# Kernel optimization log

Hardware: AMD Instinct MI355X
Metric: run time of the kernel (lower is better)

Reference implementation:

```python
import jax, jax.numpy as jnp
import numpy as np

INF = 1e38  # matches torch module's INF = 1e+38


def setup_inputs() -> dict:
    key = jax.random.key(0)
    k1, k2, k3 = jax.random.split(key, 3)
    n_len, batch, dim = 2048, 4, 512
    # scale query so QK^T logits don't fully saturate the softmax
    query = jax.random.normal(k1, (n_len, batch, dim), dtype=jnp.float32) * 0.05
    W_in = jax.random.normal(k2, (dim, dim), dtype=jnp.float32) * (1.0 / np.sqrt(dim))
    W_out = jax.random.normal(k3, (dim, 2 * dim), dtype=jnp.float32) * (1.0 / np.sqrt(2 * dim))
    return {"query": query, "W_in": W_in, "W_out": W_out}


def reference(query, W_in, W_out):
    # query: [n_len, batch, dim]; torch .t() swaps first two dims -> [batch, n_len, dim]
    q = jnp.transpose(query, (1, 0, 2))
    b, n, d = q.shape
    # attention_type == 'general': linear_in (no bias), y = x @ W^T
    q = jnp.einsum('bnd,ed->bne', q, W_in)
    # scores: [b, n, n]
    scores = jnp.einsum('bnd,bmd->bnm', q, q)
    # mask = triu(ones) INCLUDING diagonal -> set to -INF (row 0 fully masked)
    mask = jnp.triu(jnp.ones((n, n), dtype=bool))
    scores = jnp.where(mask[None, :, :], -INF, scores)
    weights = jax.nn.softmax(scores, axis=-1)  # row 0 becomes uniform (all -INF)
    # manual zero-out of row 0 of the attention weights
    weights = weights.at[:, 0, :].set(0.0)
    mix = jnp.einsum('bnm,bmd->bnd', weights, q)
    combined = jnp.concatenate([mix, q], axis=-1)  # [b, n, 2d]
    out = jnp.einsum('bnk,dk->bnd', combined, W_out)  # linear_out, no bias
    out = jax.nn.selu(out)
    # final .t() -> [n_len, batch, dim]
    return jnp.transpose(out, (1, 0, 2)), weights
```

## Files before the change

kernel.cpp:

```cpp
#include <hip/hip_runtime.h>
#include <hip/hip_bf16.h>

typedef unsigned short u16;
typedef unsigned int u32;

#define BATCH 4
#define NLEN 2048
#define DIM 512
#define LDSK 40

typedef __attribute__((ext_vector_type(8))) __bf16 bf16x8;
typedef __attribute__((ext_vector_type(4))) float f32x4;

__device__ __forceinline__ u16 f32_to_bf16(float f) {
  union { float f; u32 u; } v; v.f = f;
  u32 u = v.u;
  return (u16)((u + 0x7FFFu + ((u >> 16) & 1u)) >> 16);
}
__device__ __forceinline__ u32 pk2(float lo, float hi) {
  return (u32)f32_to_bf16(lo) | ((u32)f32_to_bf16(hi) << 16);
}
__device__ __forceinline__ void stage8_f32(u16* dst, const float* src) {
  float4 a = *(const float4*)src;
  float4 b = *(const float4*)(src + 4);
  uint4 o;
  o.x = pk2(a.x, a.y); o.y = pk2(a.z, a.w);
  o.z = pk2(b.x, b.y); o.w = pk2(b.z, b.w);
  *(uint4*)dst = o;
}
__device__ __forceinline__ void stage16_f32(u16* dst, const float* src) {
  stage8_f32(dst, src); stage8_f32(dst + 8, src + 8);
}
__device__ __forceinline__ void stage8_bf16(u16* dst, const u16* src) {
  *(uint4*)dst = *(const uint4*)src;
}
__device__ __forceinline__ void stage16_bf16(u16* dst, const u16* src) {
  *(uint4*)dst = *(const uint4*)src;
  *(uint4*)(dst + 8) = *(const uint4*)(src + 8);
}
__device__ __forceinline__ void stage8_sum(u16* dst, const u16* s0, const u16* s1,
                                           const u16* s2, int cnt) {
  uint4 a = *(const uint4*)s0;
  u32 wa[4] = {a.x, a.y, a.z, a.w};
  float v[8];
#pragma unroll
  for (int i = 0; i < 4; ++i) {
    v[2 * i] = __uint_as_float(wa[i] << 16);
    v[2 * i + 1] = __uint_as_float(wa[i] & 0xffff0000u);
  }
  if (cnt > 1) {
    uint4 bq = *(const uint4*)s1;
    u32 wb[4] = {bq.x, bq.y, bq.z, bq.w};
#pragma unroll
    for (int i = 0; i < 4; ++i) {
      v[2 * i] += __uint_as_float(wb[i] << 16);
      v[2 * i + 1] += __uint_as_float(wb[i] & 0xffff0000u);
    }
  }
  if (cnt > 2) {
    uint4 cq = *(const uint4*)s2;
    u32 wc[4] = {cq.x, cq.y, cq.z, cq.w};
#pragma unroll
    for (int i = 0; i < 4; ++i) {
      v[2 * i] += __uint_as_float(wc[i] << 16);
      v[2 * i + 1] += __uint_as_float(wc[i] & 0xffff0000u);
    }
  }
  uint4 o;
  o.x = pk2(v[0], v[1]); o.y = pk2(v[2], v[3]);
  o.z = pk2(v[4], v[5]); o.w = pk2(v[6], v[7]);
  *(uint4*)dst = o;
}

template <int MR, int NR>
__device__ __forceinline__ void mma_tile(const u16* As, const u16* Bs, f32x4 acc[MR][NR],
                                         int wm, int wn, int lr, int lk) {
  bf16x8 af[MR], bfr[NR];
#pragma unroll
  for (int m = 0; m < MR; ++m)
    af[m] = *(const bf16x8*)(As + (wm + m * 16 + lr) * LDSK + lk);
#pragma unroll
  for (int n = 0; n < NR; ++n)
    bfr[n] = *(const bf16x8*)(Bs + (wn + n * 16 + lr) * LDSK + lk);
#pragma unroll
  for (int m = 0; m < MR; ++m)
#pragma unroll
    for (int n = 0; n < NR; ++n)
      acc[m][n] = __builtin_amdgcn_mfma_f32_16x16x32_bf16(af[m], bfr[n], acc[m][n], 0, 0, 0);
}

__global__ __launch_bounds__(256) void k_qproj(const float* __restrict__ query,
                                               const float* __restrict__ W_in,
                                               u16* __restrict__ qp, u16* __restrict__ qt) {
  __shared__ u16 As[64 * LDSK];
  __shared__ u16 Bs[128 * LDSK];
  __shared__ u16 tbuf[128][72];
  const int t = threadIdx.x;
  const int lane = t & 63, wid = t >> 6;
  const int wm = (wid >> 1) * 32, wn = (wid & 1) * 64;
  const int lr = lane & 15, lk = (lane >> 4) * 8;
  const int trow4 = t >> 2, tseg = (t & 3) * 8;
  const int trow2 = t >> 1, thalf = (t & 1) * 16;
  const int rbase = blockIdx.y * 64;
  const int cbase = blockIdx.x * 128;
  const int rg = rbase + trow4;
  const int bb = rg >> 11, nn = rg & 2047;
  const float* aRow = query + (size_t)(nn * BATCH + bb) * DIM + tseg;
  const float* bRow = W_in + (size_t)(cbase + trow2) * DIM + thalf;
  f32x4 acc[2][4] = {};
  for (int k0 = 0; k0 < DIM; k0 += 32) {
    stage8_f32(As + trow4 * LDSK + tseg, aRow + k0);
    stage16_f32(Bs + trow2 * LDSK + thalf, bRow + k0);
    __syncthreads();
    mma_tile<2, 4>(As, Bs, acc, wm, wn, lr, lk);
    __syncthreads();
  }
#pragma unroll
  for (int m = 0; m < 2; ++m)
#pragma unroll
    for (int n = 0; n < 4; ++n)
#pragma unroll
      for (int j = 0; j < 4; ++j) {
        int rl = wm + m * 16 + (lane >> 4) * 4 + j;
        int cl = wn + n * 16 + lr;
        u16 v = f32_to_bf16(acc[m][n][j]);
        qp[(size_t)(rbase + rl) * DIM + cbase + cl] = v;
        tbuf[cl][rl] = v;
      }
  __syncthreads();
  const int bb0 = rbase >> 11, nbase = rbase & 2047;
#pragma unroll
  for (int i = 0; i < 4; ++i) {
    int idx = t + i * 256;
    int dl = idx >> 3, c = idx & 7;
    uint4 v = *(const uint4*)&tbuf[dl][c * 8];
    *(uint4*)(qt + (size_t)(bb0 * DIM + cbase + dl) * NLEN + nbase + c * 8) = v;
  }
}

__global__ __launch_bounds__(256) void k_scores(const u16* __restrict__ qp,
                                                u16* __restrict__ swf) {
  const int mt = blockIdx.x;
  const int nt = blockIdx.y;
  const int b = blockIdx.z;
  if (mt > (nt >> 1)) return;
  __shared__ u16 As[64 * LDSK];
  __shared__ u16 Bs[128 * LDSK];
  const int t = threadIdx.x;
  const int lane = t & 63, wid = t >> 6;
  const int wm = (wid >> 1) * 32, wn = (wid & 1) * 64;
  const int lr = lane & 15, lk = (lane >> 4) * 8;
  const int trow4 = t >> 2, tseg = (t & 3) * 8;
  const int trow2 = t >> 1, thalf = (t & 1) * 16;
  const u16* aRow = qp + (size_t)(b * NLEN + nt * 64 + trow4) * DIM + tseg;
  const u16* bRow = qp + (size_t)(b * NLEN + mt * 128 + trow2) * DIM + thalf;
  f32x4 acc[2][4] = {};
  for (int k0 = 0; k0 < DIM; k0 += 32) {
    stage8_bf16(As + trow4 * LDSK + tseg, aRow + k0);
    stage16_bf16(Bs + trow2 * LDSK + thalf, bRow + k0);
    __syncthreads();
    mma_tile<2, 4>(As, Bs, acc, wm, wn, lr, lk);
    __syncthreads();
  }
  const int NT = nt >> 1;
  u16* wtile = swf + ((size_t)(b * 136 + NT * (NT + 1) / 2 + mt) << 14);
  const int rowoff = (nt & 1) * 64;
#pragma unroll
  for (int m = 0; m < 2; ++m)
#pragma unroll
    for (int n = 0; n < 4; ++n)
#pragma unroll
      for (int j = 0; j < 4; ++j) {
        int rl = wm + m * 16 + (lane >> 4) * 4 + j;
        int cl = wn + n * 16 + lr;
        wtile[(rowoff + rl) * 128 + cl] = f32_to_bf16(acc[m][n][j]);
      }
}

__global__ __launch_bounds__(256) void k_softmax(u16* __restrict__ swf, float* __restrict__ w) {
  const int n = blockIdx.x, b = blockIdx.y;
  const int t = threadIdx.x;
  float* wrow = w + ((size_t)b * NLEN + n) * NLEN;
  const int nt = n >> 7;
  const size_t tb = ((size_t)(b * 136 + nt * (nt + 1) / 2) << 14) + ((size_t)(n & 127) << 7);
  __shared__ float srow[NLEN];
  __shared__ float red[4];
  if (n == 0) {
    for (int i = t; i < NLEN / 4; i += 256) ((float4*)wrow)[i] = float4{0, 0, 0, 0};
    if (t < 16) ((uint4*)(swf + tb))[t] = uint4{0, 0, 0, 0};
    return;
  }
  const int lane = t & 63, wid = t >> 6;
  const int nchunk = (nt + 1) * 16;
  float mx = -1e38f;
  for (int idx = t; idx < nchunk; idx += 256) {
    const int mt = idx >> 4, c = idx & 15;
    uint4 rv = *(const uint4*)(swf + tb + ((size_t)mt << 14) + c * 8);
    int m0 = mt * 128 + c * 8;
    u32 wds[4] = {rv.x, rv.y, rv.z, rv.w};
#pragma unroll
    for (int wi = 0; wi < 4; ++wi) {
      float v0 = __uint_as_float(wds[wi] << 16);
      float v1 = __uint_as_float(wds[wi] & 0xffff0000u);
      int m = m0 + wi * 2;
      srow[m] = v0; srow[m + 1] = v1;
      if (m < n) mx = fmaxf(mx, v0);
      if (m + 1 < n) mx = fmaxf(mx, v1);
    }
  }
#pragma unroll
  for (int off = 32; off; off >>= 1) mx = fmaxf(mx, __shfl_xor(mx, off));
  if (lane == 0) red[wid] = mx;
  __syncthreads();
  mx = fmaxf(fmaxf(red[0], red[1]), fmaxf(red[2], red[3]));
  float sum = 0.f;
  for (int m = t; m < n; m += 256) {
    float e = __expf(srow[m] - mx);
    srow[m] = e;
    sum += e;
  }
#pragma unroll
  for (int off = 32; off; off >>= 1) sum += __shfl_xor(sum, off);
  __syncthreads();
  if (lane == 0) red[wid] = sum;
  __syncthreads();
  float inv = 1.0f / (red[0] + red[1] + red[2] + red[3]);
  {
    int m0 = t * 8;
    float vals[8];
#pragma unroll
    for (int e = 0; e < 8; ++e) { int m = m0 + e; vals[e] = (m < n) ? srow[m] * inv : 0.f; }
    ((float4*)wrow)[t * 2] = float4{vals[0], vals[1], vals[2], vals[3]};
    ((float4*)wrow)[t * 2 + 1] = float4{vals[4], vals[5], vals[6], vals[7]};
  }
  for (int idx = t; idx < nchunk; idx += 256) {
    const int mt = idx >> 4, c = idx & 15;
    int m0 = mt * 128 + c * 8;
    u32 wo[4];
#pragma unroll
    for (int wi = 0; wi < 4; ++wi) {
      int m = m0 + wi * 2;
      float v0 = (m < n) ? srow[m] * inv : 0.f;
      float v1 = (m + 1 < n) ? srow[m + 1] * inv : 0.f;
      wo[wi] = (u32)f32_to_bf16(v0) | ((u32)f32_to_bf16(v1) << 16);
    }
    *(uint4*)(swf + tb + ((size_t)mt << 14) + c * 8) = uint4{wo[0], wo[1], wo[2], wo[3]};
  }
}

__global__ __launch_bounds__(256) void k_mix(const u16* __restrict__ swf,
                                             const u16* __restrict__ qt,
                                             u16* __restrict__ mixp) {
  const size_t PSZ = (size_t)BATCH * NLEN * DIM;
  const int bid = blockIdx.x;
  const int b = bid / 132;
  const int rem = bid % 132;
  const int dt = rem / 33;
  const int j = rem % 33;
  int nt, cp, P;
  if (j < 18) { nt = 15 - j / 3; cp = j % 3; P = 3; }
  else if (j < 28) { int jj = j - 18; nt = 9 - (jj >> 1); cp = jj & 1; P = 2; }
  else { nt = 32 - j; cp = 0; P = 1; }
  const int S = nt + 1;
  const int ks = cp * S / P, ke = (cp + 1) * S / P;
  __shared__ u16 As[128 * LDSK];
  __shared__ u16 Bs[128 * LDSK];
  const int t = threadIdx.x;
  const int lane = t & 63, wid = t >> 6;
  const int wm = (wid >> 1) * 64, wn = (wid & 1) * 64;
  const int lr = lane & 15, lk = (lane >> 4) * 8;
  const int trow2 = t >> 1, thalf = (t & 1) * 16;
  const size_t tribase = (size_t)(b * 136 + nt * (nt + 1) / 2) << 14;
  const u16* bRow = qt + (size_t)(b * DIM + dt * 128 + trow2) * NLEN + thalf;
  f32x4 acc[4][4] = {};
  for (int kstep = ks * 4; kstep < ke * 4; ++kstep) {
    const int k0 = kstep * 32;
    const int mt = k0 >> 7;
    const u16* aRow = swf + tribase + ((size_t)mt << 14) + trow2 * 128 + (k0 & 127) + thalf;
    stage16_bf16(As + trow2 * LDSK + thalf, aRow);
    stage16_bf16(Bs + trow2 * LDSK + thalf, bRow + k0);
    __syncthreads();
    mma_tile<4, 4>(As, Bs, acc, wm, wn, lr, lk);
    __syncthreads();
  }
  u16* dst = mixp + (size_t)cp * PSZ;
#pragma unroll
  for (int m = 0; m < 4; ++m)
#pragma unroll
    for (int n = 0; n < 4; ++n)
#pragma unroll
      for (int j2 = 0; j2 < 4; ++j2) {
        int row = nt * 128 + wm + m * 16 + (lane >> 4) * 4 + j2;
        int col = dt * 128 + wn + n * 16 + lr;
        dst[(size_t)(b * NLEN + row) * DIM + col] = f32_to_bf16(acc[m][n][j2]);
      }
}

__global__ __launch_bounds__(256) void k_out(const u16* __restrict__ mixp,
                                             const u16* __restrict__ qp,
                                             const float* __restrict__ W_out,
                                             float* __restrict__ out) {
  const size_t PSZ = (size_t)BATCH * NLEN * DIM;
  const int et = blockIdx.x;
  const int rt = blockIdx.y;
  __shared__ u16 As[64 * LDSK];
  __shared__ u16 Bs[64 * LDSK];
  const int t = threadIdx.x;
  const int lane = t & 63, wid = t >> 6;
  const int wm = (wid >> 1) * 32, wn = (wid & 1) * 32;
  const int lr = lane & 15, lk = (lane >> 4) * 8;
  const int trow4 = t >> 2, tseg = (t & 3) * 8;
  const int rbase = rt * 64;
  const int nt128 = (rbase & 2047) >> 7;
  const int cnt = (nt128 >= 10) ? 3 : ((nt128 >= 5) ? 2 : 1);
  const size_t arow = (size_t)(rbase + trow4) * DIM + tseg;
  const u16* m0 = mixp + arow;
  const u16* m1 = mixp + PSZ + arow;
  const u16* m2 = mixp + 2 * PSZ + arow;
  const u16* qr = qp + arow;
  const float* bRow = W_out + (size_t)(et * 64 + trow4) * (2 * DIM) + tseg;
  f32x4 acc[2][2] = {};
  for (int k0 = 0; k0 < 2 * DIM; k0 += 32) {
    if (k0 < DIM)
      stage8_sum(As + trow4 * LDSK + tseg, m0 + k0, m1 + k0, m2 + k0, cnt);
    else
      stage8_bf16(As + trow4 * LDSK + tseg, qr + (k0 - DIM));
    stage8_f32(Bs + trow4 * LDSK + tseg, bRow + k0);
    __syncthreads();
    mma_tile<2, 2>(As, Bs, acc, wm, wn, lr, lk);
    __syncthreads();
  }
  const float sc = 1.0507009873554805f;
  const float al = 1.6732632423543772f;
#pragma unroll
  for (int m = 0; m < 2; ++m)
#pragma unroll
    for (int n = 0; n < 2; ++n)
#pragma unroll
      for (int j = 0; j < 4; ++j) {
        int row = rbase + wm + m * 16 + (lane >> 4) * 4 + j;
        int col = et * 64 + wn + n * 16 + lr;
        int b2 = row >> 11, n2 = row & 2047;
        float v = acc[m][n][j];
        v = (v > 0.f) ? sc * v : sc * al * (__expf(v) - 1.f);
        out[(size_t)(n2 * BATCH + b2) * DIM + col] = v;
      }
}

extern "C" void kernel_launch(void* const* d_in, const int* in_sizes, int n_in,
                              void* d_out, int out_size, void* d_ws, size_t ws_size,
                              hipStream_t stream) {
  const float* query = (const float*)d_in[0];
  const float* W_in = (const float*)d_in[1];
  const float* W_out = (const float*)d_in[2];
  float* out0 = (float*)d_out;
  float* w = out0 + (size_t)NLEN * BATCH * DIM;

  const size_t PSZ = (size_t)BATCH * NLEN * DIM;
  u16* qp = (u16*)d_ws;
  u16* qt = qp + PSZ;
  u16* mixp = qt + PSZ;
  u16* swf = mixp + 3 * PSZ;

  dim3 blk(256);
  k_qproj<<<dim3(DIM / 128, (BATCH * NLEN) / 64), blk, 0, stream>>>(query, W_in, qp, qt);
  k_scores<<<dim3(16, 32, BATCH), blk, 0, stream>>>(qp, swf);
  k_softmax<<<dim3(NLEN, BATCH), blk, 0, stream>>>(swf, w);
  k_mix<<<dim3(528), blk, 0, stream>>>(swf, qt, mixp);
  k_out<<<dim3(8, 128), blk, 0, stream>>>(mixp, qp, W_out, out0);
}
```

Before: 154.5 us.

## Pre-reduce mix partials and pre-convert W_out, enlarge output GEMM tile

A new kernel sums the split-K mix partials into one bf16 buffer, reusing the qt workspace, and converts W_out to bf16 once. The output projection then streams plain bf16 tiles with a larger 128x64 tile and K step of 64. This removes the per-tile partial summation and float conversion that were repeated across every column block. The cost is an extra kernel launch plus one extra write and read of the summed mix and the converted weights.

```diff
diff --git a/kernel.cpp b/kernel.cpp
--- a/kernel.cpp
+++ b/kernel.cpp
@@ -8,6 +8,7 @@
 #define NLEN 2048
 #define DIM 512
 #define LDSK 40
+#define LDSB 72
 
 typedef __attribute__((ext_vector_type(8))) __bf16 bf16x8;
 typedef __attribute__((ext_vector_type(4))) float f32x4;
@@ -296,44 +297,78 @@
       }
 }
 
-__global__ __launch_bounds__(256) void k_out(const u16* __restrict__ mixp,
+__global__ __launch_bounds__(256) void k_fin(const u16* __restrict__ mixp,
+                                             u16* __restrict__ amix,
+                                             const float* __restrict__ W_out,
+                                             u16* __restrict__ wob) {
+  const size_t PSZ = (size_t)BATCH * NLEN * DIM;
+  const int bid = blockIdx.x;
+  const int t = threadIdx.x;
+  if (bid < 512) {
+#pragma unroll
+    for (int i = 0; i < 4; ++i) {
+      int g = i * 131072 + bid * 256 + t;
+      int row = g >> 6, chunk = g & 63;
+      int nt = (row & 2047) >> 7;
+      int cnt = (nt >= 10) ? 3 : ((nt >= 5) ? 2 : 1);
+      size_t off = (size_t)row * DIM + chunk * 8;
+      stage8_sum(amix + off, mixp + off, mixp + PSZ + off, mixp + 2 * PSZ + off, cnt);
+    }
+  } else {
+    int g = (bid - 512) * 256 + t;
+    stage8_f32(wob + (size_t)g * 8, W_out + (size_t)g * 8);
+  }
+}
+
+__global__ __launch_bounds__(256) void k_out(const u16* __restrict__ amix,
                                              const u16* __restrict__ qp,
-                                             const float* __restrict__ W_out,
+                                             const u16* __restrict__ wob,
                                              float* __restrict__ out) {
-  const size_t PSZ = (size_t)BATCH * NLEN * DIM;
+  __shared__ u16 As[128 * LDSB];
+  __shared__ u16 Bs[64 * LDSB];
   const int et = blockIdx.x;
   const int rt = blockIdx.y;
-  __shared__ u16 As[64 * LDSK];
-  __shared__ u16 Bs[64 * LDSK];
   const int t = threadIdx.x;
   const int lane = t & 63, wid = t >> 6;
-  const int wm = (wid >> 1) * 32, wn = (wid & 1) * 32;
+  const int wm = (wid >> 1) * 64, wn = (wid & 1) * 32;
   const int lr = lane & 15, lk = (lane >> 4) * 8;
-  const int trow4 = t >> 2, tseg = (t & 3) * 8;
-  const int rbase = rt * 64;
-  const int nt128 = (rbase & 2047) >> 7;
-  const int cnt = (nt128 >= 10) ? 3 : ((nt128 >= 5) ? 2 : 1);
-  const size_t arow = (size_t)(rbase + trow4) * DIM + tseg;
-  const u16* m0 = mixp + arow;
-  const u16* m1 = mixp + PSZ + arow;
-  const u16* m2 = mixp + 2 * PSZ + arow;
-  const u16* qr = qp + arow;
-  const float* bRow = W_out + (size_t)(et * 64 + trow4) * (2 * DIM) + tseg;
-  f32x4 acc[2][2] = {};
-  for (int k0 = 0; k0 < 2 * DIM; k0 += 32) {
-    if (k0 < DIM)
-      stage8_sum(As + trow4 * LDSK + tseg, m0 + k0, m1 + k0, m2 + k0, cnt);
-    else
-      stage8_bf16(As + trow4 * LDSK + tseg, qr + (k0 - DIM));
-    stage8_f32(Bs + trow4 * LDSK + tseg, bRow + k0);
-    __syncthreads();
-    mma_tile<2, 2>(As, Bs, acc, wm, wn, lr, lk);
+  const int rbase = rt * 128;
+  const int ar = t >> 3, ac = (t & 7) * 8;
+  const int br = t >> 2, bc = (t & 3) * 16;
+  const u16* aMix = amix + (size_t)rbase * DIM;
+  const u16* aQ = qp + (size_t)rbase * DIM;
+  const u16* bW = wob + (size_t)(et * 64 + br) * (2 * DIM) + bc;
+  f32x4 acc[4][2] = {};
+  for (int k0 = 0; k0 < 2 * DIM; k0 += 64) {
+    const u16* asrc = (k0 < DIM) ? (aMix + k0) : (aQ + (k0 - DIM));
+#pragma unroll
+    for (int i = 0; i < 4; ++i)
+      *(uint4*)(As + (ar + i * 32) * LDSB + ac) =
+          *(const uint4*)(asrc + (size_t)(ar + i * 32) * DIM + ac);
+    *(uint4*)(Bs + br * LDSB + bc) = *(const uint4*)(bW + k0);
+    *(uint4*)(Bs + br * LDSB + bc + 8) = *(const uint4*)(bW + k0 + 8);
+    __syncthreads();
+#pragma unroll
+    for (int kk = 0; kk < 64; kk += 32) {
+      bf16x8 af[4], bfr[2];
+#pragma unroll
+      for (int m = 0; m < 4; ++m)
+        af[m] = *(const bf16x8*)(As + (wm + m * 16 + lr) * LDSB + kk + lk);
+#pragma unroll
+      for (int n = 0; n < 2; ++n)
+        bfr[n] = *(const bf16x8*)(Bs + (wn + n * 16 + lr) * LDSB + kk + lk);
+#pragma unroll
+      for (int m = 0; m < 4; ++m)
+#pragma unroll
+        for (int n = 0; n < 2; ++n)
+          acc[m][n] = __builtin_amdgcn_mfma_f32_16x16x32_bf16(af[m], bfr[n], acc[m][n], 0, 0, 0);
+    }
     __syncthreads();
   }
   const float sc = 1.0507009873554805f;
   const float al = 1.6732632423543772f;
 #pragma unroll
-  for (int m = 0; m < 2; ++m)
+  for (int m = 0; m < 4; ++m)
 #pragma unroll
     for (int n = 0; n < 2; ++n)
 #pragma unroll
@@ -361,11 +396,14 @@
   u16* qt = qp + PSZ;
   u16* mixp = qt + PSZ;
   u16* swf = mixp + 3 * PSZ;
+  u16* wob = swf + (size_t)BATCH * 136 * 16384;
+  u16* amix = qt;
 
   dim3 blk(256);
   k_qproj<<<dim3(DIM / 128, (BATCH * NLEN) / 64), blk, 0, stream>>>(query, W_in, qp, qt);
   k_scores<<<dim3(16, 32, BATCH), blk, 0, stream>>>(qp, swf);
   k_softmax<<<dim3(NLEN, BATCH), blk, 0, stream>>>(swf, w);
   k_mix<<<dim3(528), blk, 0, stream>>>(swf, qt, mixp);
-  k_out<<<dim3(8, 128), blk, 0, stream>>>(mixp, qp, W_out, out0);
-}
+  k_fin<<<dim3(768), blk, 0, stream>>>(mixp, amix, W_out, wob);
+  k_out<<<dim3(8, 64), blk, 0, stream>>>(amix, qp, wob, out0);
+}
```

After: 139.5 us. 9.7% less time.
